# Kernel optimization log

Hardware: AMD Instinct MI355X
Metric: run time of the kernel (lower is better)

The kernel has to match this reference:

```python
import jax, jax.numpy as jnp
import numpy as np

D_MODEL = 1024
NUM_HEADS = 16
THETA = 10000.0


def setup_inputs() -> dict:
    key = jax.random.key(0)
    ks = jax.random.split(key, 5)
    B, S, D = 4, 2048, D_MODEL
    std = float(np.sqrt(2.0 / (D + D)))
    x = jax.random.normal(ks[0], (B, S, D), dtype=jnp.float32)
    wq = jax.random.normal(ks[1], (D, D), dtype=jnp.float32) * std
    wk = jax.random.normal(ks[2], (D, D), dtype=jnp.float32) * std
    wv = jax.random.normal(ks[3], (D, D), dtype=jnp.float32) * std
    wo = jax.random.normal(ks[4], (D, D), dtype=jnp.float32) * std
    token_positions = jnp.broadcast_to(jnp.arange(S, dtype=jnp.int32), (B, S))
    return {"x": x, "token_positions": token_positions,
            "wq": wq, "wk": wk, "wv": wv, "wo": wo}


def _rope(t, token_positions, d_k):
    # t: [B, H, S, d_k]; token_positions: [B, S]
    freqs = 1.0 / (THETA ** (jnp.arange(0, d_k, 2, dtype=jnp.float32) / d_k))  # [d_k/2]
    angles = token_positions.astype(jnp.float32)[..., None] * freqs            # [B, S, d_k/2]
    angles = jnp.repeat(angles, 2, axis=-1)                                    # [B, S, d_k]
    cos = jnp.cos(angles)[:, None, :, :]  # broadcast over heads
    sin = jnp.sin(angles)[:, None, :, :]
    t1, t2 = t[..., 0::2], t[..., 1::2]
    t_rot = jnp.stack([-t2, t1], axis=-1).reshape(t.shape)  # interleave (-x2, x1)
    return t * cos + t_rot * sin


def reference(x, token_positions, wq, wk, wv, wo):
    B, S, D = x.shape
    H = NUM_HEADS
    d_k = D // H
    def proj(w):
        return (x @ w.T).reshape(B, S, H, d_k).transpose(0, 2, 1, 3)  # [B,H,S,dk]
    q = _rope(proj(wq), token_positions, d_k)
    k = _rope(proj(wk), token_positions, d_k)
    v = proj(wv)
    scale = 1.0 / jnp.sqrt(jnp.float32(d_k))
    scores = jnp.einsum('bhqd,bhkd->bhqk', q, k) * scale  # [B,H,S,S]
    causal = jnp.tril(jnp.ones((S, S), dtype=bool))
    scores = jnp.where(causal, scores, -jnp.inf)
    attn = jax.nn.softmax(scores, axis=-1)
    out = jnp.einsum('bhqk,bhkd->bhqd', attn, v)          # [B,H,S,dk]
    out = out.transpose(0, 2, 1, 3).reshape(B, S, D)
    return out @ wo.T
```

## Files before the change

kernel.cpp:

```cpp
#include <hip/hip_runtime.h>
#include <hip/hip_bf16.h>
#include <cstdint>
#include <cstddef>

#define B_ 4
#define S_ 2048
#define D_ 1024
#define H_ 16
#define DK_ 64
#define NTOK (B_*S_)

typedef __bf16 bf16;
typedef __bf16 bf16x8 __attribute__((ext_vector_type(8)));
typedef short s16x4 __attribute__((ext_vector_type(4)));
typedef float f32x4 __attribute__((ext_vector_type(4)));

#define AS1 __attribute__((address_space(1)))
#define AS3 __attribute__((address_space(3)))

static __device__ __forceinline__ short f2bf_s(float f) {
    return __builtin_bit_cast(short, (__bf16)f);
}

static __device__ __forceinline__ f32x4 mfma16(s16x4 a, s16x4 b, f32x4 c) {
#if __has_builtin(__builtin_amdgcn_mfma_f32_16x16x16bf16_1k)
    return __builtin_amdgcn_mfma_f32_16x16x16bf16_1k(a, b, c, 0, 0, 0);
#else
    asm volatile("v_mfma_f32_16x16x16_bf16 %0, %1, %2, %0\n\ts_nop 7\n\ts_nop 7"
                 : "+v"(c) : "v"(a), "v"(b));
    return c;
#endif
}

__global__ void cvt_rope(const float* __restrict__ x, const float* __restrict__ wq,
                         const float* __restrict__ wk, const float* __restrict__ wv,
                         const float* __restrict__ wo, const int* __restrict__ pos,
                         bf16* __restrict__ dst, float2* __restrict__ tab) {
    const int NX8 = NTOK * D_ / 8;
    const int W8 = D_ * D_ / 8;
    const int NCVT = NX8 + 4 * W8;
    int i = blockIdx.x * blockDim.x + threadIdx.x;
    if (i < NCVT) {
        const float* src; int j;
        if (i < NX8) { src = x; j = i; }
        else {
            int k = i - NX8;
            int w = k >> 17;
            j = k & (W8 - 1);
            src = w == 0 ? wq : (w == 1 ? wk : (w == 2 ? wv : wo));
        }
        const float4* s4 = reinterpret_cast<const float4*>(src) + (size_t)j * 2;
        float4 a = s4[0], b = s4[1];
        bf16x8 o;
        o[0] = (bf16)a.x; o[1] = (bf16)a.y; o[2] = (bf16)a.z; o[3] = (bf16)a.w;
        o[4] = (bf16)b.x; o[5] = (bf16)b.y; o[6] = (bf16)b.z; o[7] = (bf16)b.w;
        reinterpret_cast<bf16x8*>(dst)[i] = o;
    } else {
        int k = i - NCVT;
        if (k >= NTOK * 32) return;
        int n = k >> 5, p = k & 31;
        float pf = (float)pos[n];
        float freq = powf(10000.0f, -(float)p * (1.0f / 32.0f));
        float ang = pf * freq;
        float s, c;
        sincosf(ang, &s, &c);
        tab[k] = make_float2(c, s);
    }
}

__global__ __launch_bounds__(256, 2)
void gemm_qkv(const bf16* __restrict__ A, const bf16* __restrict__ Bw,
              bf16* __restrict__ Qr, bf16* __restrict__ Kz, bf16* __restrict__ VT,
              const float2* __restrict__ tab) {
    const float SCL2E = 0.125f * 1.44269504088896340736f;
    constexpr int NKT = 16;
    __shared__ alignas(16) bf16 lds[2][(128 + 128) * 64];
    const int tid = threadIdx.x;
    const int lane = tid & 63;
    const int wid = tid >> 6;
    const int wm = wid >> 1, wn = wid & 1;
    const int lr = lane & 15, lg = lane >> 4;
    const int m0 = blockIdx.x * 128;
    const int n0g = blockIdx.y * 128;

    f32x4 acc[4][4] = {};

    auto stageA = [&](int kt, int bufi) {
        bf16* dst = &lds[bufi][0];
#pragma unroll
        for (int j = 0; j < 4; ++j) {
            int flat = j * 256 + tid;
            int r = flat >> 3, c = flat & 7;
            const bf16* src = A + (size_t)(m0 + r) * 1024 + kt * 64 + ((c ^ (r & 7)) << 3);
            __builtin_amdgcn_global_load_lds((const AS1 uint32_t*)src,
                                             (AS3 uint32_t*)(dst + (size_t)flat * 8), 16, 0, 0);
        }
    };
    auto stageB = [&](int kt, int bufi) {
        bf16* dst = &lds[bufi][0] + 128 * 64;
#pragma unroll
        for (int j = 0; j < 4; ++j) {
            int flat = j * 256 + tid;
            int r = flat >> 3, c = flat & 7;
            const bf16* src = Bw + (size_t)(n0g + r) * 1024 + kt * 64 + ((c ^ (r & 7)) << 3);
            __builtin_amdgcn_global_load_lds((const AS1 uint32_t*)src,
                                             (AS3 uint32_t*)(dst + (size_t)flat * 8), 16, 0, 0);
        }
    };

    stageA(0, 0);
    stageB(0, 0);

    for (int kt = 0; kt < NKT; ++kt) {
        const bf16* bufA = &lds[kt & 1][0];
        const bf16* bufB = bufA + 128 * 64;

        asm volatile("" ::: "memory");
        __builtin_amdgcn_s_barrier();
        asm volatile("" ::: "memory");
        if (kt + 1 < NKT) {
            stageA(kt + 1, (kt + 1) & 1);
            asm volatile("s_waitcnt vmcnt(4)" ::: "memory");
        } else {
            asm volatile("s_waitcnt vmcnt(0)" ::: "memory");
        }
        __builtin_amdgcn_s_barrier();
        asm volatile("" ::: "memory");

        const int sx = lr & 7;
        bf16x8 af[4][2], bfr[4][2];
#pragma unroll
        for (int mf = 0; mf < 4; ++mf)
#pragma unroll
            for (int kh = 0; kh < 2; ++kh)
                af[mf][kh] = *reinterpret_cast<const bf16x8*>(
                    &bufA[(wm * 64 + mf * 16 + lr) * 64 + (((kh * 4 + lg) ^ sx) << 3)]);
#pragma unroll
        for (int nf = 0; nf < 2; ++nf)
#pragma unroll
            for (int kh = 0; kh < 2; ++kh)
                bfr[nf][kh] = *reinterpret_cast<const bf16x8*>(
                    &bufB[(wn * 64 + nf * 16 + lr) * 64 + (((kh * 4 + lg) ^ sx) << 3)]);
        __builtin_amdgcn_s_setprio(1);
#pragma unroll
        for (int mf = 0; mf < 4; ++mf)
#pragma unroll
            for (int nf = 0; nf < 2; ++nf)
#pragma unroll
                for (int kh = 0; kh < 2; ++kh)
                    acc[mf][nf] = __builtin_amdgcn_mfma_f32_16x16x32_bf16(af[mf][kh], bfr[nf][kh], acc[mf][nf], 0, 0, 0);
        __builtin_amdgcn_s_setprio(0);
        if (kt + 1 < NKT) stageB(kt + 1, (kt + 1) & 1);
        asm volatile("" ::: "memory");
        __builtin_amdgcn_s_barrier();
        asm volatile("" ::: "memory");
#pragma unroll
        for (int nf = 2; nf < 4; ++nf)
#pragma unroll
            for (int kh = 0; kh < 2; ++kh)
                bfr[nf][kh] = *reinterpret_cast<const bf16x8*>(
                    &bufB[(wn * 64 + nf * 16 + lr) * 64 + (((kh * 4 + lg) ^ sx) << 3)]);
        __builtin_amdgcn_s_setprio(1);
#pragma unroll
        for (int mf = 0; mf < 4; ++mf)
#pragma unroll
            for (int nf = 2; nf < 4; ++nf)
#pragma unroll
                for (int kh = 0; kh < 2; ++kh)
                    acc[mf][nf] = __builtin_amdgcn_mfma_f32_16x16x32_bf16(af[mf][kh], bfr[nf][kh], acc[mf][nf], 0, 0, 0);
        __builtin_amdgcn_s_setprio(0);
    }

#pragma unroll
    for (int mf = 0; mf < 4; ++mf) {
#pragma unroll
        for (int nf = 0; nf < 4; ++nf) {
            int row0 = m0 + wm * 64 + mf * 16 + lg * 4;
            int colg = n0g + wn * 64 + nf * 16 + lr;
            int which = colg >> 10;
            int col = colg & 1023;
            if (which < 2) {
#pragma unroll
                for (int r = 0; r < 4; ++r) {
                    int row = row0 + r;
                    float v = acc[mf][nf][r];
                    float partner = __shfl_xor(v, 1, 64);
                    float2 cs = tab[(size_t)row * 32 + ((col >> 1) & 31)];
                    float o = (col & 1) ? fmaf(v, cs.x, partner * cs.y)
                                        : fmaf(v, cs.x, -partner * cs.y);
                    if (which == 0) {
                        Qr[(size_t)row * 1024 + col] = (bf16)(o * SCL2E);
                    } else {
                        int h = col >> 6, e = col & 63;
                        int e2 = e ^ ((row & 7) << 3);
                        Kz[(size_t)row * 1024 + h * 64 + e2] = (bf16)o;
                    }
                }
            } else {
                int h = col >> 6, dd = col & 63;
                int kvb = row0 & 63;
                int sw = (((dd & 7) ^ ((dd >> 3) & 7)) & 7) << 3;
                s16x4 pk;
#pragma unroll
                for (int r = 0; r < 4; ++r) pk[r] = f2bf_s(acc[mf][nf][r]);
                size_t addr = ((((size_t)((row0 >> 11) * 16 + h)) * 32 + ((row0 >> 6) & 31)) * 64 + dd) * 64
                              + (size_t)(kvb ^ sw);
                *reinterpret_cast<s16x4*>(&VT[addr]) = pk;
            }
        }
    }
}

__global__ __launch_bounds__(256, 2)
void gemm_out(const bf16* __restrict__ A, const bf16* __restrict__ Bw,
              float* __restrict__ Cp) {
    constexpr int NKT = 16;
    __shared__ alignas(16) bf16 lds[2][(128 + 128) * 64];
    const int tid = threadIdx.x;
    const int lane = tid & 63;
    const int wid = tid >> 6;
    const int wm = wid >> 1, wn = wid & 1;
    const int lr = lane & 15, lg = lane >> 4;
    const int m0 = blockIdx.x * 128;
    const int n0g = blockIdx.y * 128;

    f32x4 acc[4][4] = {};

    auto stageA = [&](int kt, int bufi) {
        bf16* dst = &lds[bufi][0];
#pragma unroll
        for (int j = 0; j < 4; ++j) {
            int flat = j * 256 + tid;
            int r = flat >> 3, c = flat & 7;
            const bf16* src = A + (size_t)(m0 + r) * 1024 + kt * 64 + ((c ^ (r & 7)) << 3);
            __builtin_amdgcn_global_load_lds((const AS1 uint32_t*)src,
                                             (AS3 uint32_t*)(dst + (size_t)flat * 8), 16, 0, 0);
        }
    };
    auto stageB = [&](int kt, int bufi) {
        bf16* dst = &lds[bufi][0] + 128 * 64;
#pragma unroll
        for (int j = 0; j < 4; ++j) {
            int flat = j * 256 + tid;
            int r = flat >> 3, c = flat & 7;
            const bf16* src = Bw + (size_t)(n0g + r) * 1024 + kt * 64 + ((c ^ (r & 7)) << 3);
            __builtin_amdgcn_global_load_lds((const AS1 uint32_t*)src,
                                             (AS3 uint32_t*)(dst + (size_t)flat * 8), 16, 0, 0);
        }
    };

    stageA(0, 0);
    stageB(0, 0);

    for (int kt = 0; kt < NKT; ++kt) {
        const bf16* bufA = &lds[kt & 1][0];
        const bf16* bufB = bufA + 128 * 64;

        asm volatile("" ::: "memory");
        __builtin_amdgcn_s_barrier();
        asm volatile("" ::: "memory");
        if (kt + 1 < NKT) {
            stageA(kt + 1, (kt + 1) & 1);
            asm volatile("s_waitcnt vmcnt(4)" ::: "memory");
        } else {
            asm volatile("s_waitcnt vmcnt(0)" ::: "memory");
        }
        __builtin_amdgcn_s_barrier();
        asm volatile("" ::: "memory");

        const int sx = lr & 7;
        bf16x8 af[4][2], bfr[4][2];
#pragma unroll
        for (int mf = 0; mf < 4; ++mf)
#pragma unroll
            for (int kh = 0; kh < 2; ++kh)
                af[mf][kh] = *reinterpret_cast<const bf16x8*>(
                    &bufA[(wm * 64 + mf * 16 + lr) * 64 + (((kh * 4 + lg) ^ sx) << 3)]);
#pragma unroll
        for (int nf = 0; nf < 2; ++nf)
#pragma unroll
            for (int kh = 0; kh < 2; ++kh)
                bfr[nf][kh] = *reinterpret_cast<const bf16x8*>(
                    &bufB[(wn * 64 + nf * 16 + lr) * 64 + (((kh * 4 + lg) ^ sx) << 3)]);
        __builtin_amdgcn_s_setprio(1);
#pragma unroll
        for (int mf = 0; mf < 4; ++mf)
#pragma unroll
            for (int nf = 0; nf < 2; ++nf)
#pragma unroll
                for (int kh = 0; kh < 2; ++kh)
                    acc[mf][nf] = __builtin_amdgcn_mfma_f32_16x16x32_bf16(af[mf][kh], bfr[nf][kh], acc[mf][nf], 0, 0, 0);
        __builtin_amdgcn_s_setprio(0);
        if (kt + 1 < NKT) stageB(kt + 1, (kt + 1) & 1);
        asm volatile("" ::: "memory");
        __builtin_amdgcn_s_barrier();
        asm volatile("" ::: "memory");
#pragma unroll
        for (int nf = 2; nf < 4; ++nf)
#pragma unroll
            for (int kh = 0; kh < 2; ++kh)
                bfr[nf][kh] = *reinterpret_cast<const bf16x8*>(
                    &bufB[(wn * 64 + nf * 16 + lr) * 64 + (((kh * 4 + lg) ^ sx) << 3)]);
        __builtin_amdgcn_s_setprio(1);
#pragma unroll
        for (int mf = 0; mf < 4; ++mf)
#pragma unroll
            for (int nf = 2; nf < 4; ++nf)
#pragma unroll
                for (int kh = 0; kh < 2; ++kh)
                    acc[mf][nf] = __builtin_amdgcn_mfma_f32_16x16x32_bf16(af[mf][kh], bfr[nf][kh], acc[mf][nf], 0, 0, 0);
        __builtin_amdgcn_s_setprio(0);
    }

#pragma unroll
    for (int mf = 0; mf < 4; ++mf)
#pragma unroll
        for (int nf = 0; nf < 4; ++nf)
#pragma unroll
            for (int r = 0; r < 4; ++r) {
                int row = m0 + wm * 64 + mf * 16 + lg * 4 + r;
                int colg = n0g + wn * 64 + nf * 16 + lr;
                Cp[(size_t)row * 1024 + colg] = acc[mf][nf][r];
            }
}

__global__ __launch_bounds__(256, 2)
void flash_attn16(const bf16* __restrict__ Q, const bf16* __restrict__ Kz,
                  const bf16* __restrict__ VT, bf16* __restrict__ O) {
    __shared__ bf16 Ks[2][128 * 64];
    __shared__ bf16 Vt[2][2 * 4096];
    const int tid = threadIdx.x, lane = tid & 63, w = tid >> 6;
    const int lr = lane & 15, lg = lane >> 4;
    const int qtA = blockIdx.x;
    const int qtB = 15 - qtA;
    const int q0[2] = { qtA * 128, qtB * 128 };
    const int ntS[2] = { 2 * qtA + 2, 2 * qtB + 2 };
    const int NT = ntS[1];
    const int NT2 = NT >> 1;
    const int bh = blockIdx.y;
    const int b = bh >> 4, h = bh & 15;
    const size_t base = ((size_t)b * S_) * D_ + (size_t)h * DK_;
    const size_t vtbase = (size_t)bh * 32 * 4096;

    bf16x8 aq[2][2][2];
#pragma unroll
    for (int si = 0; si < 2; ++si)
#pragma unroll
        for (int qs = 0; qs < 2; ++qs) {
            int qrow = q0[si] + w * 32 + qs * 16 + lr;
            const bf16* qp = Q + base + (size_t)qrow * D_ + lg * 8;
            aq[si][qs][0] = *reinterpret_cast<const bf16x8*>(qp);
            aq[si][qs][1] = *reinterpret_cast<const bf16x8*>(qp + 32);
        }

    f32x4 acc[2][2][4] = {};
    f32x4 l_acc[2][2] = {};

    const short ONEB = (short)0x3F80;
    const s16x4 ones = { ONEB, ONEB, ONEB, ONEB };

    const int sjj = tid >> 3;
    const int se0 = (tid & 7) * 8;

    auto stage = [&](int t2, int bufi) {
        bf16* kd = Ks[bufi];
        bf16* vd = Vt[bufi];
#pragma unroll
        for (int i = 0; i < 4; ++i) {
            int jj = sjj + i * 32;
            const bf16* ksrc = Kz + base + (size_t)(t2 * 128 + jj) * 1024 + se0;
            __builtin_amdgcn_global_load_lds((const AS1 uint32_t*)ksrc,
                                             (AS3 uint32_t*)(kd + jj * 64 + se0), 16, 0, 0);
        }
#pragma unroll
        for (int s2 = 0; s2 < 2; ++s2)
#pragma unroll
            for (int i = 0; i < 2; ++i) {
                int jj = sjj + i * 32;
                const bf16* vsrc = VT + vtbase + (size_t)(t2 * 2 + s2) * 4096 + jj * 64 + se0;
                __builtin_amdgcn_global_load_lds((const AS1 uint32_t*)vsrc,
                                                 (AS3 uint32_t*)(vd + s2 * 4096 + jj * 64 + se0), 16, 0, 0);
            }
    };

    stage(0, 0);

    for (int t2 = 0; t2 < NT2; ++t2) {
        asm volatile("" ::: "memory");
        __builtin_amdgcn_s_barrier();
        asm volatile("" ::: "memory");
        if (t2 + 1 < NT2) {
            stage(t2 + 1, (t2 + 1) & 1);
            asm volatile("s_waitcnt vmcnt(8)" ::: "memory");
        } else {
            asm volatile("s_waitcnt vmcnt(0)" ::: "memory");
        }
        __builtin_amdgcn_s_barrier();
        asm volatile("" ::: "memory");

#pragma unroll
        for (int s2 = 0; s2 < 2; ++s2) {
            const int t = t2 * 2 + s2;
            const int j0 = t * 64;
            const bf16* KsB = Ks[t2 & 1] + s2 * 64 * 64;
            const bf16* VtB = Vt[t2 & 1] + s2 * 4096;

#pragma unroll
            for (int si = 0; si < 2; ++si) {
                if (t >= ntS[si]) continue;
                const int qmaxw = q0[si] + w * 32 + 31;
                if (j0 > qmaxw) continue;

                f32x4 sc[2][4];
                __builtin_amdgcn_s_setprio(1);
#pragma unroll
                for (int nt = 0; nt < 4; ++nt) {
                    int krow = nt * 16 + lr;
                    int swz = (krow & 7) << 3;
                    bf16x8 a0 = *reinterpret_cast<const bf16x8*>(&KsB[krow * 64 + ((lg * 8) ^ swz)]);
                    bf16x8 a1 = *reinterpret_cast<const bf16x8*>(&KsB[krow * 64 + ((32 + lg * 8) ^ swz)]);
#pragma unroll
                    for (int qs = 0; qs < 2; ++qs) {
                        f32x4 tv = {};
                        tv = __builtin_amdgcn_mfma_f32_16x16x32_bf16(a0, aq[si][qs][0], tv, 0, 0, 0);
                        tv = __builtin_amdgcn_mfma_f32_16x16x32_bf16(a1, aq[si][qs][1], tv, 0, 0, 0);
                        sc[qs][nt] = tv;
                    }
                }
                __builtin_amdgcn_s_setprio(0);

                s16x4 ap[2][4];
#pragma unroll
                for (int qs = 0; qs < 2; ++qs) {
                    const int qrow = q0[si] + w * 32 + qs * 16 + lr;
                    if (j0 + 63 > q0[si] + w * 32 + qs * 16) {
#pragma unroll
                        for (int nt = 0; nt < 4; ++nt)
#pragma unroll
                            for (int r = 0; r < 4; ++r) {
                                int kv = j0 + nt * 16 + lg * 4 + r;
                                if (kv > qrow) sc[qs][nt][r] = -1e30f;
                            }
                    }
#pragma unroll
                    for (int nt = 0; nt < 4; ++nt) {
                        float p0 = exp2f(sc[qs][nt][0]);
                        float p1 = exp2f(sc[qs][nt][1]);
                        float p2 = exp2f(sc[qs][nt][2]);
                        float p3 = exp2f(sc[qs][nt][3]);
                        int ulo, uhi;
                        asm("v_cvt_pk_bf16_f32 %0, %1, %2" : "=v"(ulo) : "v"(p0), "v"(p1));
                        asm("v_cvt_pk_bf16_f32 %0, %1, %2" : "=v"(uhi) : "v"(p2), "v"(p3));
                        int2 pr; pr.x = ulo; pr.y = uhi;
                        ap[qs][nt] = __builtin_bit_cast(s16x4, pr);
                    }
                }

                __builtin_amdgcn_s_setprio(1);
#pragma unroll
                for (int qs = 0; qs < 2; ++qs)
#pragma unroll
                    for (int nt = 0; nt < 4; ++nt)
                        l_acc[si][qs] = mfma16(ap[qs][nt], ones, l_acc[si][qs]);
#pragma unroll
                for (int dt = 0; dt < 4; ++dt) {
                    int vrow = dt * 16 + lr;
                    int vswz = (((vrow & 7) ^ (vrow >> 3)) & 7) << 3;
                    s16x4 bv[4];
#pragma unroll
                    for (int nt = 0; nt < 4; ++nt)
                        bv[nt] = *reinterpret_cast<const s16x4*>(&VtB[vrow * 64 + ((nt * 16 + lg * 4) ^ vswz)]);
#pragma unroll
                    for (int qs = 0; qs < 2; ++qs)
#pragma unroll
                        for (int nt = 0; nt < 4; ++nt)
                            acc[si][qs][dt] = mfma16(ap[qs][nt], bv[nt], acc[si][qs][dt]);
                }
                __builtin_amdgcn_s_setprio(0);
            }
        }
    }

#pragma unroll
    for (int si = 0; si < 2; ++si)
#pragma unroll
        for (int qs = 0; qs < 2; ++qs)
#pragma unroll
            for (int r = 0; r < 4; ++r) {
                float invr = __builtin_amdgcn_rcpf(l_acc[si][qs][r]);
                int row = q0[si] + w * 32 + qs * 16 + lg * 4 + r;
#pragma unroll
                for (int dt = 0; dt < 4; ++dt)
                    O[base + (size_t)row * D_ + dt * 16 + lr] = (bf16)(acc[si][qs][dt][r] * invr);
            }
}

extern "C" void kernel_launch(void* const* d_in, const int* in_sizes, int n_in,
                              void* d_out, int out_size, void* d_ws, size_t ws_size,
                              hipStream_t stream) {
    const float* x  = (const float*)d_in[0];
    const int*   tp = (const int*)d_in[1];
    const float* wq = (const float*)d_in[2];
    const float* wk = (const float*)d_in[3];
    const float* wv = (const float*)d_in[4];
    const float* wo = (const float*)d_in[5];

    bf16* ws = (bf16*)d_ws;
    bf16* Xbf = ws;
    bf16* Wqb = Xbf + (size_t)NTOK * D_;
    bf16* Wkb = Wqb + (size_t)D_ * D_;
    bf16* Wvb = Wkb + (size_t)D_ * D_;
    bf16* Wob = Wvb + (size_t)D_ * D_;
    bf16* Qr  = Wob + (size_t)D_ * D_;
    bf16* Kz  = Qr + (size_t)NTOK * D_;
    bf16* VT  = Kz + (size_t)NTOK * D_;
    bf16* AO  = VT + (size_t)NTOK * D_;
    float2* tab = (float2*)(AO + (size_t)NTOK * D_);
    (void)ws_size; (void)in_sizes; (void)n_in; (void)out_size;
    (void)Wkb; (void)Wvb;

    {
        int ntot = (NTOK * D_ + 4 * D_ * D_) / 8 + NTOK * 32;
        cvt_rope<<<(ntot + 255) / 256, 256, 0, stream>>>(x, wq, wk, wv, wo, tp, Xbf, tab);
    }

    gemm_qkv<<<dim3(NTOK / 128, 24), 256, 0, stream>>>(Xbf, Wqb, Qr, Kz, VT, tab);

    flash_attn16<<<dim3(8, B_ * H_), 256, 0, stream>>>(Qr, Kz, VT, AO);

    gemm_out<<<dim3(NTOK / 128, D_ / 128), 256, 0, stream>>>(AO, Wob, (float*)d_out);
}
```

Before: 189.9 us.

## Enlarge QKV GEMM tile to 256x256 with 512-thread blocks

Rewrites the QKV projection GEMM to use 256x256 output tiles per block with 8 waves, each wave computing 128x64. Each wave now holds 8x4 accumulator fragments, and A fragments are loaded per m-row inside the MFMA loop. The split A/B staging with a mid-iteration barrier is merged into a single stage call. The goal is more data reuse per LDS byte and fewer global loads. In exchange it uses 128KB of LDS, which allows only one block per CU, and the grid shrinks to 384 blocks. Higher register pressure and less overlap between loading and compute are risks.

Result: slower. 195.2 us (+2.8%).

```diff
diff --git a/kernel.cpp b/kernel.cpp
--- a/kernel.cpp
+++ b/kernel.cpp
@@ -68,59 +68,56 @@
     }
 }
 
-__global__ __launch_bounds__(256, 2)
-void gemm_qkv(const bf16* __restrict__ A, const bf16* __restrict__ Bw,
-              bf16* __restrict__ Qr, bf16* __restrict__ Kz, bf16* __restrict__ VT,
-              const float2* __restrict__ tab) {
+__global__ __launch_bounds__(512)
+void gemm_qkv256(const bf16* __restrict__ A, const bf16* __restrict__ Bw,
+                 bf16* __restrict__ Qr, bf16* __restrict__ Kz, bf16* __restrict__ VT,
+                 const float2* __restrict__ tab) {
     const float SCL2E = 0.125f * 1.44269504088896340736f;
     constexpr int NKT = 16;
-    __shared__ alignas(16) bf16 lds[2][(128 + 128) * 64];
+    __shared__ alignas(16) bf16 lds[2][(256 + 256) * 64];
     const int tid = threadIdx.x;
     const int lane = tid & 63;
     const int wid = tid >> 6;
-    const int wm = wid >> 1, wn = wid & 1;
+    const int wm = wid >> 2;
+    const int wn = wid & 3;
     const int lr = lane & 15, lg = lane >> 4;
-    const int m0 = blockIdx.x * 128;
-    const int n0g = blockIdx.y * 128;
-
-    f32x4 acc[4][4] = {};
-
-    auto stageA = [&](int kt, int bufi) {
+    const int m0 = blockIdx.x * 256;
+    const int n0g = blockIdx.y * 256;
+
+    f32x4 acc[8][4] = {};
+
+    auto stage = [&](int kt, int bufi) {
         bf16* dst = &lds[bufi][0];
 #pragma unroll
         for (int j = 0; j < 4; ++j) {
-            int flat = j * 256 + tid;
+            int flat = j * 512 + tid;
             int r = flat >> 3, c = flat & 7;
             const bf16* src = A + (size_t)(m0 + r) * 1024 + kt * 64 + ((c ^ (r & 7)) << 3);
             __builtin_amdgcn_global_load_lds((const AS1 uint32_t*)src,
                                              (AS3 uint32_t*)(dst + (size_t)flat * 8), 16, 0, 0);
         }
-    };
-    auto stageB = [&](int kt, int bufi) {
-        bf16* dst = &lds[bufi][0] + 128 * 64;
 #pragma unroll
         for (int j = 0; j < 4; ++j) {
-            int flat = j * 256 + tid;
+            int flat = j * 512 + tid;
             int r = flat >> 3, c = flat & 7;
             const bf16* src = Bw + (size_t)(n0g + r) * 1024 + kt * 64 + ((c ^ (r & 7)) << 3);
             __builtin_amdgcn_global_load_lds((const AS1 uint32_t*)src,
-                                             (AS3 uint32_t*)(dst + (size_t)flat * 8), 16, 0, 0);
+                                             (AS3 uint32_t*)(dst + 256 * 64 + (size_t)flat * 8), 16, 0, 0);
         }
     };
 
-    stageA(0, 0);
-    stageB(0, 0);
+    stage(0, 0);
 
     for (int kt = 0; kt < NKT; ++kt) {
         const bf16* bufA = &lds[kt & 1][0];
-        const bf16* bufB = bufA + 128 * 64;
+        const bf16* bufB = bufA + 256 * 64;
 
         asm volatile("" ::: "memory");
         __builtin_amdgcn_s_barrier();
         asm volatile("" ::: "memory");
         if (kt + 1 < NKT) {
-            stageA(kt + 1, (kt + 1) & 1);
-            asm volatile("s_waitcnt vmcnt(4)" ::: "memory");
+            stage(kt + 1, (kt + 1) & 1);
+            asm volatile("s_waitcnt vmcnt(8)" ::: "memory");
         } else {
             asm volatile("s_waitcnt vmcnt(0)" ::: "memory");
         }
@@ -128,54 +125,34 @@
         asm volatile("" ::: "memory");
 
         const int sx = lr & 7;
-        bf16x8 af[4][2], bfr[4][2];
-#pragma unroll
-        for (int mf = 0; mf < 4; ++mf)
-#pragma unroll
-            for (int kh = 0; kh < 2; ++kh)
-                af[mf][kh] = *reinterpret_cast<const bf16x8*>(
-                    &bufA[(wm * 64 + mf * 16 + lr) * 64 + (((kh * 4 + lg) ^ sx) << 3)]);
-#pragma unroll
-        for (int nf = 0; nf < 2; ++nf)
+        bf16x8 bfr[4][2];
+#pragma unroll
+        for (int nf = 0; nf < 4; ++nf)
 #pragma unroll
             for (int kh = 0; kh < 2; ++kh)
                 bfr[nf][kh] = *reinterpret_cast<const bf16x8*>(
                     &bufB[(wn * 64 + nf * 16 + lr) * 64 + (((kh * 4 + lg) ^ sx) << 3)]);
         __builtin_amdgcn_s_setprio(1);
 #pragma unroll
-        for (int mf = 0; mf < 4; ++mf)
-#pragma unroll
-            for (int nf = 0; nf < 2; ++nf)
-#pragma unroll
-                for (int kh = 0; kh < 2; ++kh)
-                    acc[mf][nf] = __builtin_amdgcn_mfma_f32_16x16x32_bf16(af[mf][kh], bfr[nf][kh], acc[mf][nf], 0, 0, 0);
-        __builtin_amdgcn_s_setprio(0);
-        if (kt + 1 < NKT) stageB(kt + 1, (kt + 1) & 1);
-        asm volatile("" ::: "memory");
-        __builtin_amdgcn_s_barrier();
-        asm volatile("" ::: "memory");
-#pragma unroll
-        for (int nf = 2; nf < 4; ++nf)
-#pragma unroll
-            for (int kh = 0; kh < 2; ++kh)
-                bfr[nf][kh] = *reinterpret_cast<const bf16x8*>(
-                    &bufB[(wn * 64 + nf * 16 + lr) * 64 + (((kh * 4 + lg) ^ sx) << 3)]);
-        __builtin_amdgcn_s_setprio(1);
-#pragma unroll
-        for (int mf = 0; mf < 4; ++mf)
-#pragma unroll
-            for (int nf = 2; nf < 4; ++nf)
-#pragma unroll
-                for (int kh = 0; kh < 2; ++kh)
-                    acc[mf][nf] = __builtin_amdgcn_mfma_f32_16x16x32_bf16(af[mf][kh], bfr[nf][kh], acc[mf][nf], 0, 0, 0);
+        for (int mf = 0; mf < 8; ++mf) {
+            bf16x8 af0 = *reinterpret_cast<const bf16x8*>(
+                &bufA[(wm * 128 + mf * 16 + lr) * 64 + ((lg ^ sx) << 3)]);
+            bf16x8 af1 = *reinterpret_cast<const bf16x8*>(
+                &bufA[(wm * 128 + mf * 16 + lr) * 64 + (((4 + lg) ^ sx) << 3)]);
+#pragma unroll
+            for (int nf = 0; nf < 4; ++nf) {
+                acc[mf][nf] = __builtin_amdgcn_mfma_f32_16x16x32_bf16(af0, bfr[nf][0], acc[mf][nf], 0, 0, 0);
+                acc[mf][nf] = __builtin_amdgcn_mfma_f32_16x16x32_bf16(af1, bfr[nf][1], acc[mf][nf], 0, 0, 0);
+            }
+        }
         __builtin_amdgcn_s_setprio(0);
     }
 
 #pragma unroll
-    for (int mf = 0; mf < 4; ++mf) {
+    for (int mf = 0; mf < 8; ++mf) {
 #pragma unroll
         for (int nf = 0; nf < 4; ++nf) {
-            int row0 = m0 + wm * 64 + mf * 16 + lg * 4;
+            int row0 = m0 + wm * 128 + mf * 16 + lg * 4;
             int colg = n0g + wn * 64 + nf * 16 + lr;
             int which = colg >> 10;
             int col = colg & 1023;
@@ -524,7 +501,7 @@
         cvt_rope<<<(ntot + 255) / 256, 256, 0, stream>>>(x, wq, wk, wv, wo, tp, Xbf, tab);
     }
 
-    gemm_qkv<<<dim3(NTOK / 128, 24), 256, 0, stream>>>(Xbf, Wqb, Qr, Kz, VT, tab);
+    gemm_qkv256<<<dim3(NTOK / 256, 12), 512, 0, stream>>>(Xbf, Wqb, Qr, Kz, VT, tab);
 
     flash_attn16<<<dim3(8, B_ * H_), 256, 0, stream>>>(Qr, Kz, VT, AO);
 
```
